# Kernel tuning notes

Hardware: AMD Instinct MI355X
Metric: run time of the kernel (lower is better)

The kernel has to match this reference:

```python
import jax, jax.numpy as jnp
import numpy as np

EMB = 768
EPS = 1e-5

def setup_inputs() -> dict:
    key = jax.random.key(0)
    ks = jax.random.split(key, 7)
    B, S, D = 8, 2048, EMB
    s = 1.0 / np.sqrt(D)
    return {
        "h_": jax.random.normal(ks[0], (B, S, D), dtype=jnp.float32),
        "ln_gamma": jnp.ones((D,), jnp.float32),
        "ln_beta": jnp.zeros((D,), jnp.float32),
        "wq": jax.random.normal(ks[1], (D, D), jnp.float32) * s,
        "bq": jax.random.normal(ks[2], (D,), jnp.float32) * 0.01,
        "wk": jax.random.normal(ks[3], (D, D), jnp.float32) * s,
        "bk": jax.random.normal(ks[4], (D,), jnp.float32) * 0.01,
    }

def reference(h_, ln_gamma, ln_beta, wq, bq, wk, bk):
    # LayerNorm over last dim
    mu = jnp.mean(h_, axis=-1, keepdims=True)
    var = jnp.mean(jnp.square(h_ - mu), axis=-1, keepdims=True)
    hn = (h_ - mu) * jax.lax.rsqrt(var + EPS) * ln_gamma + ln_beta
    # Q/K projections (torch Linear: x @ W^T + b; here wq is [D_in, D_out])
    q = jnp.einsum('bsd,de->bse', hn, wq) + bq
    k = jnp.einsum('bsd,de->bse', hn, wk) + bk
    # scores: q @ k^T (no sqrt(d) scaling, matching original)
    w = jnp.einsum('bqd,bkd->bqk', q, k)
    return jax.nn.softmax(w, axis=-1)
```

## Files before the change

### kernel.cpp

```cpp
#include <hip/hip_runtime.h>
#include <stdint.h>

#define EMB   768
#define BATCH 8
#define SEQ   2048
#define ROWS  (BATCH*SEQ)
#define EPS   1e-5f

#define BM 128
#define BN 128
#define BK 32
#define BK2 64

typedef _Float16 half8 __attribute__((ext_vector_type(8)));
typedef _Float16 half4 __attribute__((ext_vector_type(4)));
typedef float    floatx4 __attribute__((ext_vector_type(4)));

__device__ __forceinline__ void g2l16(const void* g, void* l) {
    __builtin_amdgcn_global_load_lds(
        (const __attribute__((address_space(1))) unsigned int*)g,
        (__attribute__((address_space(3))) unsigned int*)l,
        16, 0, 0);
}

__global__ __launch_bounds__(256) void split_w_kernel(
    const float* __restrict__ wq, const float* __restrict__ wk,
    _Float16* __restrict__ wq_hi, _Float16* __restrict__ wq_lo,
    _Float16* __restrict__ wk_hi, _Float16* __restrict__ wk_lo)
{
    const float* src = (blockIdx.y == 0) ? wq : wk;
    _Float16* dh     = (blockIdx.y == 0) ? wq_hi : wk_hi;
    _Float16* dl     = (blockIdx.y == 0) ? wq_lo : wk_lo;
    int i4 = blockIdx.x * 256 + threadIdx.x;
    float4 v = ((const float4*)src)[i4];
    half4 vh, vl;
    float c[4] = {v.x, v.y, v.z, v.w};
#pragma unroll
    for (int t = 0; t < 4; t++) {
        _Float16 hi = (_Float16)c[t];
        vh[t] = hi;
        vl[t] = (_Float16)(c[t] - (float)hi);
    }
    ((half4*)dh)[i4] = vh;
    ((half4*)dl)[i4] = vl;
}

__global__ __launch_bounds__(256) void wtilde_kernel(
    const float* __restrict__ wk, const float* __restrict__ bq,
    float* __restrict__ wt)
{
    int row  = blockIdx.x * 4 + (threadIdx.x >> 6);
    int lane = threadIdx.x & 63;
    const float4* r4 = (const float4*)(wk + (size_t)row * EMB);
    const float4* b4 = (const float4*)bq;
    float s = 0.f;
#pragma unroll
    for (int j = 0; j < 3; j++) {
        float4 a = r4[lane + j * 64];
        float4 b = b4[lane + j * 64];
        s += a.x * b.x + a.y * b.y + a.z * b.z + a.w * b.w;
    }
#pragma unroll
    for (int sh = 1; sh < 64; sh <<= 1) s += __shfl_xor(s, sh, 64);
    if (lane == 0) wt[row] = s;
}

__global__ __launch_bounds__(256) void ln_kernel(
    const float* __restrict__ h,
    const float* __restrict__ gamma,
    const float* __restrict__ beta,
    const float* __restrict__ wt,
    _Float16* __restrict__ hn_hi,
    float* __restrict__ v_out)
{
    int row  = blockIdx.x * 4 + (threadIdx.x >> 6);
    int lane = threadIdx.x & 63;
    const float4* hr4 = (const float4*)(h + (size_t)row * EMB);
    float4 x[3];
    float s1 = 0.f, s2 = 0.f;
#pragma unroll
    for (int j = 0; j < 3; j++) {
        x[j] = hr4[lane + j * 64];
        s1 += x[j].x + x[j].y + x[j].z + x[j].w;
        s2 += x[j].x * x[j].x + x[j].y * x[j].y + x[j].z * x[j].z + x[j].w * x[j].w;
    }
#pragma unroll
    for (int s = 1; s < 64; s <<= 1) {
        s1 += __shfl_xor(s1, s, 64);
        s2 += __shfl_xor(s2, s, 64);
    }
    float mu  = s1 * (1.0f / EMB);
    float var = s2 * (1.0f / EMB) - mu * mu;
    float rs  = rsqrtf(var + EPS);
    _Float16* oh = hn_hi + (size_t)row * EMB;
    float vsum = 0.f;
#pragma unroll
    for (int j = 0; j < 3; j++) {
        int e4 = lane + j * 64;
        float4 g = ((const float4*)gamma)[e4];
        float4 b = ((const float4*)beta)[e4];
        float4 w = ((const float4*)wt)[e4];
        float v[4] = {
            (x[j].x - mu) * rs * g.x + b.x,
            (x[j].y - mu) * rs * g.y + b.y,
            (x[j].z - mu) * rs * g.z + b.z,
            (x[j].w - mu) * rs * g.w + b.w };
        vsum += v[0] * w.x + v[1] * w.y + v[2] * w.z + v[3] * w.w;
        half4 vh;
#pragma unroll
        for (int t = 0; t < 4; t++) vh[t] = (_Float16)v[t];
        *(half4*)(oh + e4 * 4) = vh;
    }
#pragma unroll
    for (int s = 1; s < 64; s <<= 1) vsum += __shfl_xor(vsum, s, 64);
    if (lane == 0) v_out[row] = vsum;
}

__global__ __launch_bounds__(256) void gt_kernel(
    const _Float16* __restrict__ wk_hi, const _Float16* __restrict__ wk_lo,
    const _Float16* __restrict__ wq_hi, const _Float16* __restrict__ wq_lo,
    _Float16* __restrict__ gt_hi, _Float16* __restrict__ gt_lo)
{
    __shared__ __attribute__((aligned(16))) _Float16 Ah_s[64 * BK];
    __shared__ __attribute__((aligned(16))) _Float16 Al_s[64 * BK];
    __shared__ __attribute__((aligned(16))) _Float16 Bh_s[64 * BK];
    __shared__ __attribute__((aligned(16))) _Float16 Bl_s[64 * BK];

    int rowbase = blockIdx.y * 64;
    int colbase = blockIdx.x * 64;
    int tid  = threadIdx.x;
    int lane = tid & 63, wave = tid >> 6;
    int wrow = (wave >> 1) * 32, wcol = (wave & 1) * 32;

    floatx4 acc[2][2];
#pragma unroll
    for (int i = 0; i < 2; i++)
#pragma unroll
        for (int j = 0; j < 2; j++) acc[i][j] = (floatx4){0.f, 0.f, 0.f, 0.f};

    size_t arow = (size_t)(rowbase + (tid >> 2)) * EMB;
    size_t brow = (size_t)(colbase + (tid >> 2)) * EMB;
    int    boff = (((tid & 3) ^ ((tid >> 3) & 3)) * 16);
    const char* gAh = (const char*)(wk_hi + arow) + boff;
    const char* gAl = (const char*)(wk_lo + arow) + boff;
    const char* gBh = (const char*)(wq_hi + brow) + boff;
    const char* gBl = (const char*)(wq_lo + brow) + boff;
    char* lAh = (char*)Ah_s + tid * 16;
    char* lAl = (char*)Al_s + tid * 16;
    char* lBh = (char*)Bh_s + tid * 16;
    char* lBl = (char*)Bl_s + tid * 16;

    for (int k0 = 0; k0 < EMB; k0 += BK) {
        __syncthreads();
        g2l16(gAh, lAh); g2l16(gAl, lAl);
        g2l16(gBh, lBh); g2l16(gBl, lBl);
        gAh += 64; gAl += 64; gBh += 64; gBl += 64;
        __syncthreads();

        half8 ah[2], al[2], bh[2], bl[2];
#pragma unroll
        for (int i = 0; i < 2; i++) {
            int roff = wrow + i * 16 + (lane & 15);
            int off = roff * 64 + ((((lane >> 4)) ^ ((roff >> 1) & 3)) * 16);
            ah[i] = *(const half8*)((const char*)Ah_s + off);
            al[i] = *(const half8*)((const char*)Al_s + off);
        }
#pragma unroll
        for (int j = 0; j < 2; j++) {
            int coff = wcol + j * 16 + (lane & 15);
            int off = coff * 64 + ((((lane >> 4)) ^ ((coff >> 1) & 3)) * 16);
            bh[j] = *(const half8*)((const char*)Bh_s + off);
            bl[j] = *(const half8*)((const char*)Bl_s + off);
        }
#pragma unroll
        for (int i = 0; i < 2; i++)
#pragma unroll
            for (int j = 0; j < 2; j++) {
                acc[i][j] = __builtin_amdgcn_mfma_f32_16x16x32_f16(ah[i], bh[j], acc[i][j], 0, 0, 0);
                acc[i][j] = __builtin_amdgcn_mfma_f32_16x16x32_f16(ah[i], bl[j], acc[i][j], 0, 0, 0);
                acc[i][j] = __builtin_amdgcn_mfma_f32_16x16x32_f16(al[i], bh[j], acc[i][j], 0, 0, 0);
            }
    }

#pragma unroll
    for (int j = 0; j < 2; j++) {
        int col = colbase + wcol + j * 16 + (lane & 15);
#pragma unroll
        for (int i = 0; i < 2; i++) {
#pragma unroll
            for (int r = 0; r < 4; r++) {
                int row = rowbase + wrow + i * 16 + (lane >> 4) * 4 + r;
                float v = acc[i][j][r];
                _Float16 hi = (_Float16)v;
                gt_hi[(size_t)row * EMB + col] = hi;
                gt_lo[(size_t)row * EMB + col] = (_Float16)(v - (float)hi);
            }
        }
    }
}

__global__ __launch_bounds__(256) void t_kernel(
    const _Float16* __restrict__ hn_hi,
    const _Float16* __restrict__ gt_hi, const _Float16* __restrict__ gt_lo,
    _Float16* __restrict__ t_hi)
{
    __shared__ __attribute__((aligned(16))) _Float16 Ah_s[BM * BK2];
    __shared__ __attribute__((aligned(16))) _Float16 Bh_s[BN * BK2];
    __shared__ __attribute__((aligned(16))) _Float16 Bl_s[BN * BK2];

    int id  = (int)blockIdx.y * 6 + (int)blockIdx.x;
    int vid = (id & 7) * 96 + (id >> 3);
    int by  = vid / 6;
    int bx  = vid % 6;

    int rowbase = by * BM;
    int colbase = bx * BN;
    int tid  = threadIdx.x;
    int lane = tid & 63, wave = tid >> 6;
    int wrow = (wave >> 1) * 64, wcol = (wave & 1) * 64;

    floatx4 acc[4][4];
#pragma unroll
    for (int i = 0; i < 4; i++)
#pragma unroll
        for (int j = 0; j < 4; j++) acc[i][j] = (floatx4){0.f, 0.f, 0.f, 0.f};

    size_t arow = (size_t)(rowbase + tid / 8) * EMB;
    size_t brow = (size_t)(colbase + tid / 8) * EMB;
    int    boff = (((tid % 8) ^ ((tid >> 3) & 7)) * 16);
    const char* gAh = (const char*)(hn_hi + arow) + boff;
    const char* gBh = (const char*)(gt_hi + brow) + boff;
    const char* gBl = (const char*)(gt_lo + brow) + boff;
    char* lAh = (char*)Ah_s + tid * 16;
    char* lBh = (char*)Bh_s + tid * 16;
    char* lBl = (char*)Bl_s + tid * 16;
    const size_t pstride = (size_t)32 * EMB * 2;

    for (int k0 = 0; k0 < EMB; k0 += BK2) {
        __syncthreads();
#pragma unroll
        for (int p = 0; p < 4; p++) {
            g2l16(gAh + p * pstride, lAh + p * 4096);
            g2l16(gBh + p * pstride, lBh + p * 4096);
            g2l16(gBl + p * pstride, lBl + p * 4096);
        }
        gAh += 128; gBh += 128; gBl += 128;
        __syncthreads();

#pragma unroll
        for (int ko = 0; ko < 2; ko++) {
            half8 ah[4], bh[4], bl[4];
#pragma unroll
            for (int i = 0; i < 4; i++) {
                int roff = wrow + i * 16 + (lane & 15);
                int off = roff * 128 + ((ko * 64 + (lane >> 4) * 16) ^ ((roff & 7) << 4));
                ah[i] = *(const half8*)((const char*)Ah_s + off);
            }
#pragma unroll
            for (int j = 0; j < 4; j++) {
                int coff = wcol + j * 16 + (lane & 15);
                int off = coff * 128 + ((ko * 64 + (lane >> 4) * 16) ^ ((coff & 7) << 4));
                bh[j] = *(const half8*)((const char*)Bh_s + off);
                bl[j] = *(const half8*)((const char*)Bl_s + off);
            }
#pragma unroll
            for (int i = 0; i < 4; i++)
#pragma unroll
                for (int j = 0; j < 4; j++) {
                    acc[i][j] = __builtin_amdgcn_mfma_f32_16x16x32_f16(ah[i], bh[j], acc[i][j], 0, 0, 0);
                    acc[i][j] = __builtin_amdgcn_mfma_f32_16x16x32_f16(ah[i], bl[j], acc[i][j], 0, 0, 0);
                }
        }
    }

#pragma unroll
    for (int j = 0; j < 4; j++) {
        int col = colbase + wcol + j * 16 + (lane & 15);
#pragma unroll
        for (int i = 0; i < 4; i++) {
#pragma unroll
            for (int r = 0; r < 4; r++) {
                int row = rowbase + wrow + i * 16 + (lane >> 4) * 4 + r;
                t_hi[(size_t)row * EMB + col] = (_Float16)acc[i][j][r];
            }
        }
    }
}

template<bool F16OUT>
__global__ __launch_bounds__(256) void scores_kernel(
    const _Float16* __restrict__ t_hi,
    const _Float16* __restrict__ hn_hi,
    const float* __restrict__ v_in,
    float* __restrict__ out,
    _Float16* __restrict__ pt,
    float2* __restrict__ state)
{
    __shared__ __attribute__((aligned(16))) _Float16 Ah_s[2][BM * BK2];
    __shared__ __attribute__((aligned(16))) _Float16 Bh_s[2][BN * BK2];
    __shared__ float red[128][2];

    int b = blockIdx.z;
    size_t base = (size_t)b * SEQ * EMB;
    int rowbase = blockIdx.y * BM;
    int colbase = blockIdx.x * BN;
    int tid  = threadIdx.x;
    int lane = tid & 63, wave = tid >> 6;
    int wrow = (wave >> 1) * 64, wcol = (wave & 1) * 64;

    floatx4 acc[4][4];
#pragma unroll
    for (int i = 0; i < 4; i++)
#pragma unroll
        for (int j = 0; j < 4; j++) acc[i][j] = (floatx4){0.f, 0.f, 0.f, 0.f};

    size_t arow = base + (size_t)(rowbase + tid / 8) * EMB;
    size_t brow = base + (size_t)(colbase + tid / 8) * EMB;
    int    boff = (((tid % 8) ^ ((tid >> 3) & 7)) * 16);
    const char* gAh = (const char*)(t_hi + arow) + boff;
    const char* gBh = (const char*)(hn_hi + brow) + boff;
    char* lAh0 = (char*)Ah_s[0] + tid * 16;
    char* lBh0 = (char*)Bh_s[0] + tid * 16;
    char* lAh1 = (char*)Ah_s[1] + tid * 16;
    char* lBh1 = (char*)Bh_s[1] + tid * 16;
    const size_t pstride = (size_t)32 * EMB * 2;

    auto STAGE = [&](int c) {
        char* lA = c ? lAh1 : lAh0;
        char* lB = c ? lBh1 : lBh0;
#pragma unroll
        for (int p = 0; p < 4; p++) {
            g2l16(gAh + p * pstride, lA + p * 4096);
            g2l16(gBh + p * pstride, lB + p * 4096);
        }
        gAh += 128; gBh += 128;
    };

    const int NT = EMB / BK2;
    STAGE(0);
#pragma unroll 2
    for (int t = 0; t < NT; t++) {
        int cur = t & 1;
        asm volatile("" ::: "memory");
        if (t < NT - 1) {
            STAGE(cur ^ 1);
            asm volatile("s_waitcnt vmcnt(8)" ::: "memory");
        } else {
            asm volatile("s_waitcnt vmcnt(0)" ::: "memory");
        }
        __builtin_amdgcn_s_barrier();
        asm volatile("" ::: "memory");

#pragma unroll
        for (int ko = 0; ko < 2; ko++) {
            half8 ah[4], bh[4];
#pragma unroll
            for (int i = 0; i < 4; i++) {
                int roff = wrow + i * 16 + (lane & 15);
                int off = roff * 128 + ((ko * 64 + (lane >> 4) * 16) ^ ((roff & 7) << 4));
                ah[i] = *(const half8*)((const char*)Ah_s[cur] + off);
            }
#pragma unroll
            for (int j = 0; j < 4; j++) {
                int coff = wcol + j * 16 + (lane & 15);
                int off = coff * 128 + ((ko * 64 + (lane >> 4) * 16) ^ ((coff & 7) << 4));
                bh[j] = *(const half8*)((const char*)Bh_s[cur] + off);
            }
#pragma unroll
            for (int i = 0; i < 4; i++)
#pragma unroll
                for (int j = 0; j < 4; j++)
                    acc[i][j] = __builtin_amdgcn_mfma_f32_16x16x32_f16(ah[i], bh[j], acc[i][j], 0, 0, 0);
        }
        asm volatile("" ::: "memory");
        __builtin_amdgcn_s_barrier();
    }

    const float* vb = v_in + (size_t)b * SEQ + colbase;
#pragma unroll
    for (int j = 0; j < 4; j++) {
        float vv = vb[wcol + j * 16 + (lane & 15)];
#pragma unroll
        for (int i = 0; i < 4; i++)
#pragma unroll
            for (int r = 0; r < 4; r++) acc[i][j][r] += vv;
    }

    float m1[4][4];
#pragma unroll
    for (int i = 0; i < 4; i++)
#pragma unroll
        for (int r = 0; r < 4; r++) {
            float m = fmaxf(fmaxf(acc[i][0][r], acc[i][1][r]), fmaxf(acc[i][2][r], acc[i][3][r]));
#pragma unroll
            for (int s = 1; s < 16; s <<= 1) m = fmaxf(m, __shfl_xor(m, s, 64));
            m1[i][r] = m;
        }
    if ((lane & 15) == 0) {
#pragma unroll
        for (int i = 0; i < 4; i++)
#pragma unroll
            for (int r = 0; r < 4; r++)
                red[wrow + i * 16 + (lane >> 4) * 4 + r][wave & 1] = m1[i][r];
    }
    __syncthreads();
    float mrow[4][4];
#pragma unroll
    for (int i = 0; i < 4; i++)
#pragma unroll
        for (int r = 0; r < 4; r++) {
            int rr = wrow + i * 16 + (lane >> 4) * 4 + r;
            mrow[i][r] = fmaxf(red[rr][0], red[rr][1]);
        }
    __syncthreads();

    float ls[4][4];
#pragma unroll
    for (int i = 0; i < 4; i++)
#pragma unroll
        for (int r = 0; r < 4; r++) {
            float s = 0.f;
#pragma unroll
            for (int j = 0; j < 4; j++) {
                float e = __expf(acc[i][j][r] - mrow[i][r]);
                acc[i][j][r] = e;
                s += e;
            }
#pragma unroll
            for (int sh = 1; sh < 16; sh <<= 1) s += __shfl_xor(s, sh, 64);
            ls[i][r] = s;
        }
    if ((lane & 15) == 0) {
#pragma unroll
        for (int i = 0; i < 4; i++)
#pragma unroll
            for (int r = 0; r < 4; r++)
                red[wrow + i * 16 + (lane >> 4) * 4 + r][wave & 1] = ls[i][r];
    }
    __syncthreads();

    size_t outbase = (size_t)b * SEQ * SEQ;
#pragma unroll
    for (int i = 0; i < 4; i++)
#pragma unroll
        for (int j = 0; j < 4; j++)
#pragma unroll
            for (int r = 0; r < 4; r++) {
                int row = rowbase + wrow + i * 16 + (lane >> 4) * 4 + r;
                int col = colbase + wcol + j * 16 + (lane & 15);
                if (F16OUT)
                    pt[outbase + (size_t)row * SEQ + col] = (_Float16)acc[i][j][r];
                else
                    out[outbase + (size_t)row * SEQ + col] = acc[i][j][r];
            }

    if ((wave & 1) == 0 && (lane & 15) == 0) {
#pragma unroll
        for (int i = 0; i < 4; i++)
#pragma unroll
            for (int r = 0; r < 4; r++) {
                int rr = wrow + i * 16 + (lane >> 4) * 4 + r;
                float l = red[rr][0] + red[rr][1];
                state[((size_t)b * SEQ + rowbase + rr) * 16 + blockIdx.x] =
                    make_float2(mrow[i][r], l);
            }
    }
}

template<bool F16IN>
__global__ __launch_bounds__(256) void fixup_kernel(
    float* __restrict__ out,
    const _Float16* __restrict__ pt,
    const float2* __restrict__ state)
{
    int row  = blockIdx.x * 4 + (threadIdx.x >> 6);
    int lane = threadIdx.x & 63;
    float2 v = state[(size_t)row * 16 + (lane & 15)];
    float M = v.x;
#pragma unroll
    for (int s = 1; s < 16; s <<= 1) M = fmaxf(M, __shfl_xor(M, s, 64));
    float e  = __expf(v.x - M);
    float Lp = v.y * e;
#pragma unroll
    for (int s = 1; s < 16; s <<= 1) Lp += __shfl_xor(Lp, s, 64);
    float fv = e / Lp;

    if (F16IN) {
        const half8* p8 = (const half8*)(pt + (size_t)row * SEQ);
        float4* o4 = (float4*)(out + (size_t)row * SEQ);
#pragma unroll
        for (int c0 = 0; c0 < 4; c0++) {
            int i8 = c0 * 64 + lane;
            float s = __shfl(fv, i8 >> 4, 64);
            half8 h = p8[i8];
            float4 a, bqv;
            a.x = (float)h[0] * s; a.y = (float)h[1] * s;
            a.z = (float)h[2] * s; a.w = (float)h[3] * s;
            bqv.x = (float)h[4] * s; bqv.y = (float)h[5] * s;
            bqv.z = (float)h[6] * s; bqv.w = (float)h[7] * s;
            o4[i8 * 2]     = a;
            o4[i8 * 2 + 1] = bqv;
        }
    } else {
        float4* o4 = (float4*)(out + (size_t)row * SEQ);
#pragma unroll
        for (int c0 = 0; c0 < 8; c0++) {
            int i4 = c0 * 64 + lane;
            float s = __shfl(fv, i4 >> 5, 64);
            float4 w = o4[i4];
            w.x *= s; w.y *= s; w.z *= s; w.w *= s;
            o4[i4] = w;
        }
    }
}

extern "C" void kernel_launch(void* const* d_in, const int* in_sizes, int n_in,
                              void* d_out, int out_size, void* d_ws, size_t ws_size,
                              hipStream_t stream)
{
    const float* h  = (const float*)d_in[0];
    const float* g  = (const float*)d_in[1];
    const float* be = (const float*)d_in[2];
    const float* wq = (const float*)d_in[3];
    const float* bq = (const float*)d_in[4];
    const float* wk = (const float*)d_in[5];
    const float* bk = (const float*)d_in[6];
    (void)bk;
    float* out = (float*)d_out;

    char* ws = (char*)d_ws;
    const size_t SZ  = (size_t)ROWS * EMB * 2;
    const size_t WSZ = (size_t)EMB * EMB * 2;
    _Float16* hn_hi = (_Float16*)(ws);
    _Float16* t_hi  = (_Float16*)(ws + SZ);
    char* wbase = ws + 2 * SZ;
    _Float16* wq_hi = (_Float16*)(wbase);
    _Float16* wq_lo = (_Float16*)(wbase + WSZ);
    _Float16* wk_hi = (_Float16*)(wbase + 2 * WSZ);
    _Float16* wk_lo = (_Float16*)(wbase + 3 * WSZ);
    _Float16* gt_hi = (_Float16*)(wbase + 4 * WSZ);
    _Float16* gt_lo = (_Float16*)(wbase + 5 * WSZ);
    char* sbase = wbase + 6 * WSZ;
    float*  wt = (float*)(sbase);
    float*  v  = (float*)(sbase + 4096);
    float2* st = (float2*)(sbase + 4096 + 65536);
    char*   ptb = sbase + 4096 + 65536 + (size_t)ROWS * 16 * sizeof(float2);
    const size_t PTSZ = (size_t)BATCH * SEQ * SEQ * 2;
    _Float16* pt = (_Float16*)ptb;
    bool use_f16 = ws_size >= (size_t)(ptb - ws) + PTSZ;

    split_w_kernel<<<dim3(576, 2), 256, 0, stream>>>(wq, wk, wq_hi, wq_lo, wk_hi, wk_lo);
    wtilde_kernel<<<dim3(EMB / 4), 256, 0, stream>>>(wk, bq, wt);
    ln_kernel<<<dim3(ROWS / 4), 256, 0, stream>>>(h, g, be, wt, hn_hi, v);
    gt_kernel<<<dim3(EMB / 64, EMB / 64), 256, 0, stream>>>(wk_hi, wk_lo, wq_hi, wq_lo, gt_hi, gt_lo);
    t_kernel<<<dim3(EMB / BN, ROWS / BM), 256, 0, stream>>>(hn_hi, gt_hi, gt_lo, t_hi);
    if (use_f16) {
        scores_kernel<true><<<dim3(SEQ / BN, SEQ / BM, BATCH), 256, 0, stream>>>(t_hi, hn_hi, v, out, pt, st);
        fixup_kernel<true><<<dim3(ROWS / 4), 256, 0, stream>>>(out, pt, st);
    } else {
        scores_kernel<false><<<dim3(SEQ / BN, SEQ / BM, BATCH), 256, 0, stream>>>(t_hi, hn_hi, v, out, nullptr, st);
        fixup_kernel<false><<<dim3(ROWS / 4), 256, 0, stream>>>(out, nullptr, st);
    }
}
```

Before: 352.3 us.

## Concatenate G hi/lo along K and double-buffer t_kernel LDS loads

The gt_kernel output now stores the hi and lo halves side by side in one 1536-wide matrix. t_kernel treats them as a single K=1536 reduction and re-reads the A tile (hn_hi) for the lo half. t_kernel also gains a two-stage LDS double buffer that issues the next tile's async global-to-LDS loads before computing the current one, using explicit vmcnt waits and barriers. This is meant to hide load latency and cut LDS traffic per step, at the cost of doubled A loads and more LDS per block.

```diff
diff --git a/kernel.cpp b/kernel.cpp
--- a/kernel.cpp
+++ b/kernel.cpp
@@ -119,7 +119,7 @@
 __global__ __launch_bounds__(256) void gt_kernel(
     const _Float16* __restrict__ wk_hi, const _Float16* __restrict__ wk_lo,
     const _Float16* __restrict__ wq_hi, const _Float16* __restrict__ wq_lo,
-    _Float16* __restrict__ gt_hi, _Float16* __restrict__ gt_lo)
+    _Float16* __restrict__ gt_cat)
 {
     __shared__ __attribute__((aligned(16))) _Float16 Ah_s[64 * BK];
     __shared__ __attribute__((aligned(16))) _Float16 Al_s[64 * BK];
@@ -192,8 +192,8 @@
                 int row = rowbase + wrow + i * 16 + (lane >> 4) * 4 + r;
                 float v = acc[i][j][r];
                 _Float16 hi = (_Float16)v;
-                gt_hi[(size_t)row * EMB + col] = hi;
-                gt_lo[(size_t)row * EMB + col] = (_Float16)(v - (float)hi);
+                gt_cat[(size_t)row * 1536 + col]       = hi;
+                gt_cat[(size_t)row * 1536 + 768 + col] = (_Float16)(v - (float)hi);
             }
         }
     }
@@ -201,12 +201,11 @@
 
 __global__ __launch_bounds__(256) void t_kernel(
     const _Float16* __restrict__ hn_hi,
-    const _Float16* __restrict__ gt_hi, const _Float16* __restrict__ gt_lo,
+    const _Float16* __restrict__ gt_cat,
     _Float16* __restrict__ t_hi)
 {
-    __shared__ __attribute__((aligned(16))) _Float16 Ah_s[BM * BK2];
-    __shared__ __attribute__((aligned(16))) _Float16 Bh_s[BN * BK2];
-    __shared__ __attribute__((aligned(16))) _Float16 Bl_s[BN * BK2];
+    __shared__ __attribute__((aligned(16))) _Float16 Ah_s[2][BM * BK2];
+    __shared__ __attribute__((aligned(16))) _Float16 Bh_s[2][BN * BK2];
 
     int id  = (int)blockIdx.y * 6 + (int)blockIdx.x;
     int vid = (id & 7) * 96 + (id >> 3);
@@ -226,51 +225,63 @@
         for (int j = 0; j < 4; j++) acc[i][j] = (floatx4){0.f, 0.f, 0.f, 0.f};
 
     size_t arow = (size_t)(rowbase + tid / 8) * EMB;
-    size_t brow = (size_t)(colbase + tid / 8) * EMB;
+    size_t brow = (size_t)(colbase + tid / 8) * 1536;
     int    boff = (((tid % 8) ^ ((tid >> 3) & 7)) * 16);
-    const char* gAh = (const char*)(hn_hi + arow) + boff;
-    const char* gBh = (const char*)(gt_hi + brow) + boff;
-    const char* gBl = (const char*)(gt_lo + brow) + boff;
-    char* lAh = (char*)Ah_s + tid * 16;
-    char* lBh = (char*)Bh_s + tid * 16;
-    char* lBl = (char*)Bl_s + tid * 16;
-    const size_t pstride = (size_t)32 * EMB * 2;
-
-    for (int k0 = 0; k0 < EMB; k0 += BK2) {
-        __syncthreads();
+    const char* gA0 = (const char*)(hn_hi + arow) + boff;
+    const char* gB0 = (const char*)(gt_cat + brow) + boff;
+    const size_t pstrideA = (size_t)32 * EMB * 2;
+    const size_t pstrideB = (size_t)32 * 1536 * 2;
+
+    auto STAGE = [&](int c, int kt) {
+        const char* ga = gA0 + (kt % 12) * 128;
+        const char* gb = gB0 + kt * 128;
+        char* lA = (char*)Ah_s[c] + tid * 16;
+        char* lB = (char*)Bh_s[c] + tid * 16;
 #pragma unroll
         for (int p = 0; p < 4; p++) {
-            g2l16(gAh + p * pstride, lAh + p * 4096);
-            g2l16(gBh + p * pstride, lBh + p * 4096);
-            g2l16(gBl + p * pstride, lBl + p * 4096);
-        }
-        gAh += 128; gBh += 128; gBl += 128;
-        __syncthreads();
+            g2l16(ga + p * pstrideA, lA + p * 4096);
+            g2l16(gb + p * pstrideB, lB + p * 4096);
+        }
+    };
+
+    const int NT = (2 * EMB) / BK2;
+    STAGE(0, 0);
+#pragma unroll 2
+    for (int t = 0; t < NT; t++) {
+        int cur = t & 1;
+        asm volatile("" ::: "memory");
+        if (t < NT - 1) {
+            STAGE(cur ^ 1, t + 1);
+            asm volatile("s_waitcnt vmcnt(8)" ::: "memory");
+        } else {
+            asm volatile("s_waitcnt vmcnt(0)" ::: "memory");
+        }
+        __builtin_amdgcn_s_barrier();
+        asm volatile("" ::: "memory");
 
 #pragma unroll
         for (int ko = 0; ko < 2; ko++) {
-            half8 ah[4], bh[4], bl[4];
+            half8 ah[4], bh[4];
 #pragma unroll
             for (int i = 0; i < 4; i++) {
                 int roff = wrow + i * 16 + (lane & 15);
                 int off = roff * 128 + ((ko * 64 + (lane >> 4) * 16) ^ ((roff & 7) << 4));
-                ah[i] = *(const half8*)((const char*)Ah_s + off);
+                ah[i] = *(const half8*)((const char*)Ah_s[cur] + off);
             }
 #pragma unroll
             for (int j = 0; j < 4; j++) {
                 int coff = wcol + j * 16 + (lane & 15);
                 int off = coff * 128 + ((ko * 64 + (lane >> 4) * 16) ^ ((coff & 7) << 4));
-                bh[j] = *(const half8*)((const char*)Bh_s + off);
-                bl[j] = *(const half8*)((const char*)Bl_s + off);
+                bh[j] = *(const half8*)((const char*)Bh_s[cur] + off);
             }
 #pragma unroll
             for (int i = 0; i < 4; i++)
 #pragma unroll
-                for (int j = 0; j < 4; j++) {
+                for (int j = 0; j < 4; j++)
                     acc[i][j] = __builtin_amdgcn_mfma_f32_16x16x32_f16(ah[i], bh[j], acc[i][j], 0, 0, 0);
-                    acc[i][j] = __builtin_amdgcn_mfma_f32_16x16x32_f16(ah[i], bl[j], acc[i][j], 0, 0, 0);
-                }
-        }
+        }
+        asm volatile("" ::: "memory");
+        __builtin_amdgcn_s_barrier();
     }
 
 #pragma unroll
@@ -538,8 +549,7 @@
     _Float16* wq_lo = (_Float16*)(wbase + WSZ);
     _Float16* wk_hi = (_Float16*)(wbase + 2 * WSZ);
     _Float16* wk_lo = (_Float16*)(wbase + 3 * WSZ);
-    _Float16* gt_hi = (_Float16*)(wbase + 4 * WSZ);
-    _Float16* gt_lo = (_Float16*)(wbase + 5 * WSZ);
+    _Float16* gt_cat = (_Float16*)(wbase + 4 * WSZ);
     char* sbase = wbase + 6 * WSZ;
     float*  wt = (float*)(sbase);
     float*  v  = (float*)(sbase + 4096);
@@ -552,8 +562,8 @@
     split_w_kernel<<<dim3(576, 2), 256, 0, stream>>>(wq, wk, wq_hi, wq_lo, wk_hi, wk_lo);
     wtilde_kernel<<<dim3(EMB / 4), 256, 0, stream>>>(wk, bq, wt);
     ln_kernel<<<dim3(ROWS / 4), 256, 0, stream>>>(h, g, be, wt, hn_hi, v);
-    gt_kernel<<<dim3(EMB / 64, EMB / 64), 256, 0, stream>>>(wk_hi, wk_lo, wq_hi, wq_lo, gt_hi, gt_lo);
-    t_kernel<<<dim3(EMB / BN, ROWS / BM), 256, 0, stream>>>(hn_hi, gt_hi, gt_lo, t_hi);
+    gt_kernel<<<dim3(EMB / 64, EMB / 64), 256, 0, stream>>>(wk_hi, wk_lo, wq_hi, wq_lo, gt_cat);
+    t_kernel<<<dim3(EMB / BN, ROWS / BM), 256, 0, stream>>>(hn_hi, gt_cat, t_hi);
     if (use_f16) {
         scores_kernel<true><<<dim3(SEQ / BN, SEQ / BM, BATCH), 256, 0, stream>>>(t_hi, hn_hi, v, out, pt, st);
         fixup_kernel<true><<<dim3(ROWS / 4), 256, 0, stream>>>(out, pt, st);
```

Measured after the change: 354.7 us. About the same (+0.7%).
